# Performance work log

Hardware: AMD Instinct MI355X
Metric: run time of the kernel (lower is better)

Reference implementation:

```python
import jax, jax.numpy as jnp
import numpy as np

N = 50000
E = 400000
IN_DIM = 128
HID = 128
OUT = 128
HEADS = 8
NEG_SLOPE = 0.2  # PyG GATConv default
BN_EPS = 1e-5


def _gat_conv(x, W, a_src, a_dst, b, src, dst, concat):
    """PyG GATConv (eval): self-loops added by caller. x:[N,F], W:[F,H*C], a_*:[H,C]."""
    H, C = a_src.shape
    xW = (x @ W).reshape(N, H, C)                       # [N,H,C]
    es = jnp.sum(xW * a_src[None], axis=-1)             # [N,H]
    ed = jnp.sum(xW * a_dst[None], axis=-1)             # [N,H]
    e = jax.nn.leaky_relu(es[src] + ed[dst], NEG_SLOPE) # [E,H]
    m = jax.ops.segment_max(e, dst, num_segments=N)     # softmax over incoming edges per dst
    ex = jnp.exp(e - m[dst])
    denom = jax.ops.segment_sum(ex, dst, num_segments=N)
    alpha = ex / denom[dst]                             # [E,H]
    out = jax.ops.segment_sum(xW[src] * alpha[:, :, None], dst, num_segments=N)  # [N,H,C]
    out = out.reshape(N, H * C) if concat else out.mean(axis=1)
    return out + b


def _bn_eval(h, g, be, rm, rv):
    return (h - rm) * jax.lax.rsqrt(rv + BN_EPS) * g + be


def setup_inputs() -> dict:
    key = jax.random.key(0)
    ks = jax.random.split(key, 20)
    C1 = HID // HEADS
    f32 = jnp.float32
    inp = {
        "x": jax.random.normal(ks[0], (N, IN_DIM), dtype=f32),
        "edge_index": jax.random.randint(ks[1], (2, E), 0, N, dtype=jnp.int64),
        # GAT layer 1 (in->hid, 8 heads, concat)
        "W1": jax.random.normal(ks[2], (IN_DIM, HEADS * C1), dtype=f32) * 0.05,
        "a_src1": jax.random.normal(ks[3], (HEADS, C1), dtype=f32) * 0.05,
        "a_dst1": jax.random.normal(ks[4], (HEADS, C1), dtype=f32) * 0.05,
        "b1": jnp.zeros((HEADS * C1,), dtype=f32),
        # GAT layer 2 (hid->hid, 8 heads, concat)
        "W2": jax.random.normal(ks[5], (HID, HEADS * C1), dtype=f32) * 0.05,
        "a_src2": jax.random.normal(ks[6], (HEADS, C1), dtype=f32) * 0.05,
        "a_dst2": jax.random.normal(ks[7], (HEADS, C1), dtype=f32) * 0.05,
        "b2": jnp.zeros((HEADS * C1,), dtype=f32),
        # GAT layer 3 (hid->out, 1 head, no concat)
        "W3": jax.random.normal(ks[8], (HID, OUT), dtype=f32) * 0.05,
        "a_src3": jax.random.normal(ks[9], (1, OUT), dtype=f32) * 0.05,
        "a_dst3": jax.random.normal(ks[10], (1, OUT), dtype=f32) * 0.05,
        "b3": jnp.zeros((OUT,), dtype=f32),
        # residual linears
        "R1w": jax.random.normal(ks[11], (IN_DIM, HID), dtype=f32) * 0.05,
        "R1b": jnp.zeros((HID,), dtype=f32),
        "R2w": jax.random.normal(ks[12], (HID, HID), dtype=f32) * 0.05,
        "R2b": jnp.zeros((HID,), dtype=f32),
        "R3w": jax.random.normal(ks[13], (HID, OUT), dtype=f32) * 0.05,
        "R3b": jnp.zeros((OUT,), dtype=f32),
        # batch norms (eval mode: running stats)
        "g1": jnp.ones((HID,), dtype=f32), "be1": jnp.zeros((HID,), dtype=f32),
        "rm1": jnp.zeros((HID,), dtype=f32), "rv1": jnp.ones((HID,), dtype=f32),
        "g2": jnp.ones((HID,), dtype=f32), "be2": jnp.zeros((HID,), dtype=f32),
        "rm2": jnp.zeros((HID,), dtype=f32), "rv2": jnp.ones((HID,), dtype=f32),
    }
    return inp


def reference(x, edge_index, W1, a_src1, a_dst1, b1, W2, a_src2, a_dst2, b2,
              W3, a_src3, a_dst3, b3, R1w, R1b, R2w, R2b, R3w, R3b,
              g1, be1, rm1, rv1, g2, be2, rm2, rv2):
    # PyG GATConv adds self-loops by default
    loops = jnp.arange(N, dtype=edge_index.dtype)
    src = jnp.concatenate([edge_index[0], loops])
    dst = jnp.concatenate([edge_index[1], loops])

    h = _gat_conv(x, W1, a_src1, a_dst1, b1, src, dst, concat=True) + (x @ R1w + R1b)
    h1 = jax.nn.relu(_bn_eval(h, g1, be1, rm1, rv1))  # dropout identity in eval

    h = _gat_conv(h1, W2, a_src2, a_dst2, b2, src, dst, concat=True) + (h1 @ R2w + R2b)
    h2 = jax.nn.relu(_bn_eval(h, g2, be2, rm2, rv2))

    out = _gat_conv(h2, W3, a_src3, a_dst3, b3, src, dst, concat=False) + (h2 @ R3w + R3b)
    return out
```

## Files before the change

### kernel.cpp

```cpp
#include <hip/hip_runtime.h>
#include <hip/hip_bf16.h>
#include <type_traits>

typedef __hip_bfloat16 bf16;
typedef __hip_bfloat162 bf162;
typedef short v8s __attribute__((ext_vector_type(8)));
typedef short v4s __attribute__((ext_vector_type(4)));
typedef float v4f __attribute__((ext_vector_type(4)));

#define CAP 64

__device__ __forceinline__ float lrelu(float x) { return x > 0.f ? x : 0.2f * x; }
__device__ __forceinline__ float b2f(bf16 v) { return __bfloat162float(v); }

__global__ void k_preW(const float* __restrict__ s0, const float* __restrict__ s1,
                       const float* __restrict__ s2, const float* __restrict__ s3,
                       const float* __restrict__ s4, const float* __restrict__ s5,
                       const float* __restrict__ as1, const float* __restrict__ ad1,
                       const float* __restrict__ as2, const float* __restrict__ ad2,
                       const float* __restrict__ as3, const float* __restrict__ ad3,
                       const float* b1, const float* R1b, const float* g1, const float* be1,
                       const float* rm1, const float* rv1,
                       const float* b2, const float* R2b, const float* g2, const float* be2,
                       const float* rm2, const float* rv2,
                       const float* b3, const float* R3b,
                       bf16* __restrict__ wt, float* __restrict__ prm,
                       int* __restrict__ cnt, int N) {
    int b = blockIdx.x;
    int t = threadIdx.x;
    if (b >= 7) {
        int n4 = N * 4;
        int base = ((b - 7) * 256 + t) * 4;
        int4 z = {0, 0, 0, 0};
#pragma unroll
        for (int k = 0; k < 4; ++k)
            if (base + k < n4) ((int4*)cnt)[base + k] = z;
        return;
    }
    if (b == 6) {
        int c = t;
        if (c < 128) {
            float s1v = g1[c] * rsqrtf(rv1[c] + 1e-5f);
            prm[c]       = b1[c] + R1b[c];
            prm[128 + c] = s1v;
            prm[256 + c] = be1[c] - rm1[c] * s1v;
            float s2v = g2[c] * rsqrtf(rv2[c] + 1e-5f);
            prm[384 + c] = b2[c] + R2b[c];
            prm[512 + c] = s2v;
            prm[640 + c] = be2[c] - rm2[c] * s2v;
            prm[768 + c] = b3[c] + R3b[c];
        }
        return;
    }
    const float* src;
    switch (b) {
        case 0: src = s0; break; case 1: src = s1; break; case 2: src = s2; break;
        case 3: src = s3; break; case 4: src = s4; break; default: src = s5; break;
    }
    bf16* dst = wt + (size_t)b * 18432;
    for (int i = t; i < 16384; i += 256) {
        int k = i >> 7, n = i & 127;
        dst[n * 128 + k] = __float2bfloat16(src[i]);
    }
    if ((b & 1) == 0) {
        int layer = b >> 1;
        if (layer < 2) {
            const float* asr = (layer == 0) ? as1 : as2;
            const float* ads = (layer == 0) ? ad1 : ad2;
            for (int i = t; i < 2048; i += 256) {
                int row = i >> 7, k = i & 127, h = row & 7;
                const float* av = (row < 8) ? asr : ads;
                float s = 0.f;
#pragma unroll
                for (int c = 0; c < 16; ++c) s += src[k * 128 + h * 16 + c] * av[h * 16 + c];
                dst[(128 + row) * 128 + k] = __float2bfloat16(s);
            }
        } else {
            for (int i = t; i < 2048; i += 256) {
                int row = i >> 7, k = i & 127;
                float s = 0.f;
                if (row == 0 || row == 8) {
                    const float* av = (row == 0) ? as3 : ad3;
                    for (int c = 0; c < 128; ++c) s += src[k * 128 + c] * av[c];
                }
                dst[(128 + row) * 128 + k] = __float2bfloat16(s);
            }
        }
    } else {
        for (int i = t; i < 2048; i += 256)
            dst[16384 + i] = __float2bfloat16(0.f);
    }
}

template <typename T>
__device__ __forceinline__ void gemm_body(const T* __restrict__ A,
                                          const bf16* __restrict__ BT0, const bf16* __restrict__ BT1,
                                          bf16* __restrict__ O0, bf16* __restrict__ O1,
                                          float* __restrict__ esed, float* __restrict__ es,
                                          float* __restrict__ ed,
                                          int mode, int nrows, int job, int ntiles,
                                          bf16* Bsh) {
    const int y = (job >= ntiles) ? 1 : 0;
    const int tile = y ? job - ntiles : job;
    const bf16* BT = y ? BT1 : BT0;
    bf16* O = y ? O1 : O0;
    const int t = threadIdx.x;
    const int rowbase = tile * 128;
    const int wave = t >> 6, lane = t & 63, quad = lane >> 4, l16 = lane & 15;

    int gr[2], gc[2];
    gr[0] = rowbase + wave * 32 + l16; gc[0] = gr[0] < nrows ? gr[0] : nrows - 1;
    gr[1] = gr[0] + 16;                gc[1] = gr[1] < nrows ? gr[1] : nrows - 1;
    v8s afr[2][4];
    if constexpr (std::is_same<T, float>::value) {
#pragma unroll
        for (int rt = 0; rt < 2; ++rt) {
            const float* ar = A + (size_t)gc[rt] * 128 + quad * 8;
#pragma unroll
            for (int kit = 0; kit < 4; ++kit) {
                float4 u = *(const float4*)(ar + kit * 32);
                float4 w = *(const float4*)(ar + kit * 32 + 4);
                union { bf16 h[8]; v8s v; } tmp;
                tmp.h[0] = __float2bfloat16(u.x); tmp.h[1] = __float2bfloat16(u.y);
                tmp.h[2] = __float2bfloat16(u.z); tmp.h[3] = __float2bfloat16(u.w);
                tmp.h[4] = __float2bfloat16(w.x); tmp.h[5] = __float2bfloat16(w.y);
                tmp.h[6] = __float2bfloat16(w.z); tmp.h[7] = __float2bfloat16(w.w);
                afr[rt][kit] = tmp.v;
            }
        }
    } else {
#pragma unroll
        for (int rt = 0; rt < 2; ++rt) {
            const bf16* ar = A + (size_t)gc[rt] * 128 + quad * 8;
#pragma unroll
            for (int kit = 0; kit < 4; ++kit)
                afr[rt][kit] = *(const v8s*)(ar + kit * 32);
        }
    }

    for (int s = t; s < 288; s += 256) {
        int r = s >> 1, hf = s & 1;
        const float4* bsrc = (const float4*)(BT + r * 128 + hf * 64);
#pragma unroll
        for (int j = 0; j < 8; ++j) {
            int c = hf * 8 + j, cp = c ^ (r & 7);
            *(float4*)(&Bsh[r * 128 + cp * 8]) = bsrc[j];
        }
    }
    __syncthreads();

    v4f acc[2][9];
#pragma unroll
    for (int i = 0; i < 2; ++i)
#pragma unroll
        for (int j = 0; j < 9; ++j) acc[i][j] = (v4f){0.f, 0.f, 0.f, 0.f};
#pragma unroll
    for (int kit = 0; kit < 4; ++kit) {
        v8s bfr[9];
#pragma unroll
        for (int ct = 0; ct < 9; ++ct) {
            int nn = ct * 16 + l16;
            int cp = (kit * 4 + quad) ^ (nn & 7);
            bfr[ct] = *(const v8s*)(&Bsh[nn * 128 + cp * 8]);
        }
#pragma unroll
        for (int rt = 0; rt < 2; ++rt)
#pragma unroll
            for (int ct = 0; ct < 9; ++ct)
                acc[rt][ct] = __builtin_amdgcn_mfma_f32_16x16x32_bf16(bfr[ct], afr[rt][kit], acc[rt][ct], 0, 0, 0);
    }

#pragma unroll
    for (int rt = 0; rt < 2; ++rt) {
        if (gr[rt] < nrows) {
            bf16* orow = O + (size_t)gr[rt] * 128 + quad * 4;
#pragma unroll
            for (int ct = 0; ct < 8; ++ct) {
                union { bf16 h[4]; v4s v; } pk;
#pragma unroll
                for (int r = 0; r < 4; ++r) pk.h[r] = __float2bfloat16(acc[rt][ct][r]);
                *(v4s*)(orow + ct * 16) = pk.v;
            }
            if (mode == 1 && y == 0) {
                *(v4f*)(esed + (size_t)gr[rt] * 16 + quad * 4) = acc[rt][8];
            } else if (mode == 2 && y == 0) {
                if (quad == 0) es[gr[rt]] = acc[rt][8][0];
                else if (quad == 2) ed[gr[rt]] = acc[rt][8][0];
            }
        }
    }
}

__global__ void k_fillgemm(const float* __restrict__ A,
                           const bf16* __restrict__ BT0, const bf16* __restrict__ BT1,
                           bf16* __restrict__ O0, bf16* __restrict__ O1,
                           float* __restrict__ esed, float* __restrict__ es, float* __restrict__ ed,
                           int nrows, int ntiles, int fb,
                           const int* __restrict__ ei, int* __restrict__ cnt,
                           int* __restrict__ csr, int E) {
    __shared__ bf16 Bsh[144 * 128];
    const int nb = 2 * ntiles + fb;
    const int b = blockIdx.x;
    const int f0 = (int)(((long)b * fb) / nb);
    const int f1 = (int)(((long)(b + 1) * fb) / nb);
    if (f1 > f0) {
        int base = f0 * 1024 + threadIdx.x * 4;
        if (base >= E) return;
        if (((E & 3) == 0) && base + 3 < E) {
            int4 s4 = *(const int4*)(ei + base);
            int4 d4 = *(const int4*)(ei + E + base);
            int p0 = atomicAdd(&cnt[(size_t)d4.x * 16], 1);
            int p1 = atomicAdd(&cnt[(size_t)d4.y * 16], 1);
            int p2 = atomicAdd(&cnt[(size_t)d4.z * 16], 1);
            int p3 = atomicAdd(&cnt[(size_t)d4.w * 16], 1);
            if (p0 < CAP) csr[d4.x * CAP + p0] = s4.x;
            if (p1 < CAP) csr[d4.y * CAP + p1] = s4.y;
            if (p2 < CAP) csr[d4.z * CAP + p2] = s4.z;
            if (p3 < CAP) csr[d4.w * CAP + p3] = s4.w;
        } else {
            for (int i = base; i < E && i < base + 4; ++i) {
                int d = ei[E + i];
                int pos = atomicAdd(&cnt[(size_t)d * 16], 1);
                if (pos < CAP) csr[d * CAP + pos] = ei[i];
            }
        }
        return;
    }
    gemm_body<float>(A, BT0, BT1, O0, O1, esed, es, ed, 1, nrows, b - f0, ntiles, Bsh);
}

__global__ void k_gemm(const bf16* __restrict__ A,
                       const bf16* __restrict__ BT0, const bf16* __restrict__ BT1,
                       bf16* __restrict__ O0, bf16* __restrict__ O1,
                       float* __restrict__ esed, float* __restrict__ es, float* __restrict__ ed,
                       int mode, int nrows, int ntiles) {
    __shared__ bf16 Bsh[144 * 128];
    gemm_body<bf16>(A, BT0, BT1, O0, O1, esed, es, ed, mode, nrows, blockIdx.x, ntiles, Bsh);
}

__global__ void k_agg8(const bf16* __restrict__ xW, const float* __restrict__ esed,
                       const int* __restrict__ cnt, const int* __restrict__ csr,
                       const bf16* __restrict__ rres, const float* __restrict__ prm,
                       bf16* __restrict__ hout, int n) {
    int wave = threadIdx.x >> 6, lane = threadIdx.x & 63;
    int node = blockIdx.x * 4 + wave;
    if (node >= n) return;
    const int g = lane >> 4, l16 = lane & 15;
    const int c0 = l16 * 8;
    const int hc = l16 >> 1;
    const int he = lane & 7;
    float edw = esed[(size_t)node * 16 + 8 + he];
    float wselfh = __expf(lrelu(esed[(size_t)node * 16 + he] + edw));
    float acc[8]; float den = 0.f;
    v8s rv;
#pragma unroll
    for (int i = 0; i < 8; ++i) acc[i] = 0.f;
    {
        float ws = __shfl(wselfh, hc);
        if (g == 0) {
            rv = *(const v8s*)(rres + (size_t)node * 128 + c0);
            v8s xv = *(const v8s*)(xW + (size_t)node * 128 + c0);
            const bf16* xb = (const bf16*)&xv;
            den = ws;
#pragma unroll
            for (int i = 0; i < 8; ++i) acc[i] = ws * b2f(xb[i]);
        }
    }
    int deg = cnt[(size_t)node * 16]; if (deg > CAP) deg = CAP;
    const int* bucket = csr + (size_t)node * CAP;
    int idx = (lane < deg) ? bucket[lane] : node;
    for (int sub = 0; sub * 8 < deg; ++sub) {
        int j0 = sub * 8 + g, j1 = sub * 8 + 4 + g;
        int sv0 = __shfl(idx, j0);
        int sv1 = __shfl(idx, j1);
        v8s xv0 = *(const v8s*)(xW + (size_t)sv0 * 128 + c0);
        v8s xv1 = *(const v8s*)(xW + (size_t)sv1 * 128 + c0);
        int e = sub * 8 + (lane >> 3);
        int sidx = __shfl(idx, e);
        float esv = esed[(size_t)sidx * 16 + he];
        float w = (e < deg) ? __expf(lrelu(esv + edw)) : 0.f;
        float w0 = __shfl(w, g * 8 + hc);
        float w1 = __shfl(w, (4 + g) * 8 + hc);
        const bf16* xb0 = (const bf16*)&xv0;
        const bf16* xb1 = (const bf16*)&xv1;
        den += w0 + w1;
#pragma unroll
        for (int i = 0; i < 8; ++i) acc[i] += w0 * b2f(xb0[i]) + w1 * b2f(xb1[i]);
    }
    den += __shfl_xor(den, 16); den += __shfl_xor(den, 32);
#pragma unroll
    for (int i = 0; i < 8; ++i) {
        acc[i] += __shfl_xor(acc[i], 16);
        acc[i] += __shfl_xor(acc[i], 32);
    }
    if (g == 0) {
        float inv = 1.f / den;
        const bf16* rb = (const bf16*)&rv;
        bf16 outv[8];
#pragma unroll
        for (int i = 0; i < 8; ++i) {
            int c = c0 + i;
            float v = acc[i] * inv + prm[c] + b2f(rb[i]);
            v = fmaxf(v * prm[128 + c] + prm[256 + c], 0.f);
            outv[i] = __float2bfloat16(v);
        }
        *(v8s*)(hout + (size_t)node * 128 + c0) = *(v8s*)outv;
    }
}

__global__ void k_agg1(const bf16* __restrict__ xW, const float* __restrict__ es,
                       const float* __restrict__ ed,
                       const int* __restrict__ cnt, const int* __restrict__ csr,
                       const bf16* __restrict__ rres, const float* __restrict__ bias,
                       float* __restrict__ out, int n) {
    int wave = threadIdx.x >> 6, lane = threadIdx.x & 63;
    int node = blockIdx.x * 4 + wave;
    if (node >= n) return;
    const int g = lane >> 4, l16 = lane & 15;
    const int c0 = l16 * 8;
    float edv = ed[node];
    float wself = __expf(lrelu(es[node] + edv));
    float acc[8]; float den = 0.f;
    v8s rv;
#pragma unroll
    for (int i = 0; i < 8; ++i) acc[i] = 0.f;
    if (g == 0) {
        rv = *(const v8s*)(rres + (size_t)node * 128 + c0);
        v8s xv = *(const v8s*)(xW + (size_t)node * 128 + c0);
        const bf16* xb = (const bf16*)&xv;
        den = wself;
#pragma unroll
        for (int i = 0; i < 8; ++i) acc[i] = wself * b2f(xb[i]);
    }
    int deg = cnt[(size_t)node * 16]; if (deg > CAP) deg = CAP;
    const int* bucket = csr + (size_t)node * CAP;
    int idx = (lane < deg) ? bucket[lane] : node;
    float w = (lane < deg) ? __expf(lrelu(es[idx] + edv)) : 0.f;
    for (int j = 0; j < deg; j += 4) {
        int jl = j + g;
        int sv = __shfl(idx, jl);
        float wj = __shfl(w, jl);
        if (jl >= deg) wj = 0.f;
        v8s xv = *(const v8s*)(xW + (size_t)sv * 128 + c0);
        const bf16* xb = (const bf16*)&xv;
        den += wj;
#pragma unroll
        for (int i = 0; i < 8; ++i) acc[i] += wj * b2f(xb[i]);
    }
    den += __shfl_xor(den, 16); den += __shfl_xor(den, 32);
#pragma unroll
    for (int i = 0; i < 8; ++i) {
        acc[i] += __shfl_xor(acc[i], 16);
        acc[i] += __shfl_xor(acc[i], 32);
    }
    if (g == 0) {
        float inv = 1.f / den;
        const bf16* rb = (const bf16*)&rv;
        float ov[8];
#pragma unroll
        for (int i = 0; i < 8; ++i)
            ov[i] = acc[i] * inv + bias[c0 + i] + b2f(rb[i]);
        float4 o0, o1;
        o0.x = ov[0]; o0.y = ov[1]; o0.z = ov[2]; o0.w = ov[3];
        o1.x = ov[4]; o1.y = ov[5]; o1.z = ov[6]; o1.w = ov[7];
        *(float4*)(out + (size_t)node * 128 + c0) = o0;
        *(float4*)(out + (size_t)node * 128 + c0 + 4) = o1;
    }
}

extern "C" void kernel_launch(void* const* d_in, const int* in_sizes, int n_in,
                              void* d_out, int out_size, void* d_ws, size_t ws_size,
                              hipStream_t stream) {
    const float* x   = (const float*)d_in[0];
    const int*   ei  = (const int*)d_in[1];
    const float* W1  = (const float*)d_in[2];
    const float* as1 = (const float*)d_in[3];
    const float* ad1 = (const float*)d_in[4];
    const float* b1  = (const float*)d_in[5];
    const float* W2  = (const float*)d_in[6];
    const float* as2 = (const float*)d_in[7];
    const float* ad2 = (const float*)d_in[8];
    const float* b2  = (const float*)d_in[9];
    const float* W3  = (const float*)d_in[10];
    const float* as3 = (const float*)d_in[11];
    const float* ad3 = (const float*)d_in[12];
    const float* b3  = (const float*)d_in[13];
    const float* R1w = (const float*)d_in[14];
    const float* R1b = (const float*)d_in[15];
    const float* R2w = (const float*)d_in[16];
    const float* R2b = (const float*)d_in[17];
    const float* R3w = (const float*)d_in[18];
    const float* R3b = (const float*)d_in[19];
    const float* g1  = (const float*)d_in[20];
    const float* be1 = (const float*)d_in[21];
    const float* rm1 = (const float*)d_in[22];
    const float* rv1 = (const float*)d_in[23];
    const float* g2  = (const float*)d_in[24];
    const float* be2 = (const float*)d_in[25];
    const float* rm2 = (const float*)d_in[26];
    const float* rv2 = (const float*)d_in[27];

    const int N = in_sizes[0] / 128;
    const int E = in_sizes[1] / 2;

    char* p = (char*)d_ws;
    size_t off = 0;
    auto alloc = [&](size_t b) { void* r = p + off; off = (off + b + 255) & ~(size_t)255; return r; };
    int*   cnt  = (int*)alloc((size_t)N * 16 * 4);
    int*   csr  = (int*)alloc((size_t)N * CAP * 4);
    bf16*  WT   = (bf16*)alloc((size_t)6 * 18432 * 2);
    float* prm  = (float*)alloc(896 * 4);
    float* esed = (float*)alloc((size_t)N * 16 * 4);
    float* es   = (float*)alloc((size_t)N * 4);
    float* ed   = (float*)alloc((size_t)N * 4);
    bf16*  xW   = (bf16*)alloc((size_t)N * 128 * 2);
    bf16*  rres = (bf16*)alloc((size_t)N * 128 * 2);
    bf16*  hA   = (bf16*)alloc((size_t)N * 128 * 2);
    bf16*  hB   = (bf16*)alloc((size_t)N * 128 * 2);
    (void)ws_size; (void)n_in; (void)out_size;

    const int gx = (N + 127) / 128;
    const int nw = (N + 3) / 4;
    const int fb = (E + 1023) / 1024;
    const int zb = (N * 4 + 1023) / 1024;

    k_preW<<<7 + zb, 256, 0, stream>>>(W1, R1w, W2, R2w, W3, R3w,
                                       as1, ad1, as2, ad2, as3, ad3,
                                       b1, R1b, g1, be1, rm1, rv1,
                                       b2, R2b, g2, be2, rm2, rv2, b3, R3b,
                                       WT, prm, cnt, N);
    k_fillgemm<<<2 * gx + fb, 256, 0, stream>>>(x, WT, WT + 18432, xW, rres, esed, es, ed,
                                                N, gx, fb, ei, cnt, csr, E);
    k_agg8<<<nw, 256, 0, stream>>>(xW, esed, cnt, csr, rres, prm, hA, N);
    k_gemm<<<2 * gx, 256, 0, stream>>>(hA, WT + 2 * 18432, WT + 3 * 18432, xW, rres, esed, es, ed, 1, N, gx);
    k_agg8<<<nw, 256, 0, stream>>>(xW, esed, cnt, csr, rres, prm + 384, hB, N);
    k_gemm<<<2 * gx, 256, 0, stream>>>(hB, WT + 4 * 18432, WT + 5 * 18432, xW, rres, esed, es, ed, 2, N, gx);
    k_agg1<<<nw, 256, 0, stream>>>(xW, es, ed, cnt, csr, rres, prm + 768, (float*)d_out, N);
}
```

Baseline: 335.0 us.

## Stage GEMM output through LDS for coalesced row stores; reorder fill/gemm blocks

```diff
diff --git a/kernel.cpp b/kernel.cpp
--- a/kernel.cpp
+++ b/kernel.cpp
@@ -170,17 +170,41 @@
                 acc[rt][ct] = __builtin_amdgcn_mfma_f32_16x16x32_bf16(bfr[ct], afr[rt][kit], acc[rt][ct], 0, 0, 0);
     }
 
+    __syncthreads();
+
+    bf16* Tw = Bsh + wave * 4096;
+#pragma unroll
+    for (int rt = 0; rt < 2; ++rt) {
+        bf16* trow = Tw + (rt * 16 + l16) * 128;
+#pragma unroll
+        for (int ct = 0; ct < 8; ++ct) {
+            union { bf16 h[4]; v4s v; } pk;
+#pragma unroll
+            for (int r = 0; r < 4; ++r) pk.h[r] = __float2bfloat16(acc[rt][ct][r]);
+            int e = (ct * 16 + quad * 4 + l16 * 8) & 127;
+            *(v4s*)(trow + e) = pk.v;
+        }
+    }
+#pragma unroll
+    for (int o = 0; o < 2; ++o) {
+        int r32 = o * 16 + (lane >> 2);
+        int q4 = lane & 3;
+        int grow = rowbase + wave * 32 + r32;
+        const bf16* trow = Tw + r32 * 128;
+        int rot = (r32 & 15) * 8;
+        if (grow < nrows) {
+            bf16* orow = O + (size_t)grow * 128;
+#pragma unroll
+            for (int j = 0; j < 4; ++j) {
+                int c = q4 * 8 + j * 32;
+                int pc = (c + rot) & 127;
+                *(float4*)(orow + c) = *(const float4*)(trow + pc);
+            }
+        }
+    }
 #pragma unroll
     for (int rt = 0; rt < 2; ++rt) {
         if (gr[rt] < nrows) {
-            bf16* orow = O + (size_t)gr[rt] * 128 + quad * 4;
-#pragma unroll
-            for (int ct = 0; ct < 8; ++ct) {
-                union { bf16 h[4]; v4s v; } pk;
-#pragma unroll
-                for (int r = 0; r < 4; ++r) pk.h[r] = __float2bfloat16(acc[rt][ct][r]);
-                *(v4s*)(orow + ct * 16) = pk.v;
-            }
             if (mode == 1 && y == 0) {
                 *(v4f*)(esed + (size_t)gr[rt] * 16 + quad * 4) = acc[rt][8];
             } else if (mode == 2 && y == 0) {
@@ -195,38 +219,35 @@
                            const bf16* __restrict__ BT0, const bf16* __restrict__ BT1,
                            bf16* __restrict__ O0, bf16* __restrict__ O1,
                            float* __restrict__ esed, float* __restrict__ es, float* __restrict__ ed,
-                           int nrows, int ntiles, int fb,
+                           int nrows, int ntiles,
                            const int* __restrict__ ei, int* __restrict__ cnt,
                            int* __restrict__ csr, int E) {
-    __shared__ bf16 Bsh[144 * 128];
-    const int nb = 2 * ntiles + fb;
-    const int b = blockIdx.x;
-    const int f0 = (int)(((long)b * fb) / nb);
-    const int f1 = (int)(((long)(b + 1) * fb) / nb);
-    if (f1 > f0) {
-        int base = f0 * 1024 + threadIdx.x * 4;
-        if (base >= E) return;
-        if (((E & 3) == 0) && base + 3 < E) {
-            int4 s4 = *(const int4*)(ei + base);
-            int4 d4 = *(const int4*)(ei + E + base);
-            int p0 = atomicAdd(&cnt[(size_t)d4.x * 16], 1);
-            int p1 = atomicAdd(&cnt[(size_t)d4.y * 16], 1);
-            int p2 = atomicAdd(&cnt[(size_t)d4.z * 16], 1);
-            int p3 = atomicAdd(&cnt[(size_t)d4.w * 16], 1);
-            if (p0 < CAP) csr[d4.x * CAP + p0] = s4.x;
-            if (p1 < CAP) csr[d4.y * CAP + p1] = s4.y;
-            if (p2 < CAP) csr[d4.z * CAP + p2] = s4.z;
-            if (p3 < CAP) csr[d4.w * CAP + p3] = s4.w;
-        } else {
-            for (int i = base; i < E && i < base + 4; ++i) {
-                int d = ei[E + i];
-                int pos = atomicAdd(&cnt[(size_t)d * 16], 1);
-                if (pos < CAP) csr[d * CAP + pos] = ei[i];
-            }
-        }
+    __shared__ __align__(16) bf16 Bsh[144 * 128];
+    const int njobs = 2 * ntiles;
+    if (blockIdx.x < njobs) {
+        gemm_body<float>(A, BT0, BT1, O0, O1, esed, es, ed, 1, nrows, blockIdx.x, ntiles, Bsh);
         return;
     }
-    gemm_body<float>(A, BT0, BT1, O0, O1, esed, es, ed, 1, nrows, b - f0, ntiles, Bsh);
+    int base = (blockIdx.x - njobs) * 1024 + threadIdx.x * 4;
+    if (base >= E) return;
+    if (((E & 3) == 0) && base + 3 < E) {
+        int4 s4 = *(const int4*)(ei + base);
+        int4 d4 = *(const int4*)(ei + E + base);
+        int p0 = atomicAdd(&cnt[(size_t)d4.x * 16], 1);
+        int p1 = atomicAdd(&cnt[(size_t)d4.y * 16], 1);
+        int p2 = atomicAdd(&cnt[(size_t)d4.z * 16], 1);
+        int p3 = atomicAdd(&cnt[(size_t)d4.w * 16], 1);
+        if (p0 < CAP) csr[d4.x * CAP + p0] = s4.x;
+        if (p1 < CAP) csr[d4.y * CAP + p1] = s4.y;
+        if (p2 < CAP) csr[d4.z * CAP + p2] = s4.z;
+        if (p3 < CAP) csr[d4.w * CAP + p3] = s4.w;
+    } else {
+        for (int i = base; i < E && i < base + 4; ++i) {
+            int d = ei[E + i];
+            int pos = atomicAdd(&cnt[(size_t)d * 16], 1);
+            if (pos < CAP) csr[d * CAP + pos] = ei[i];
+        }
+    }
 }
 
 __global__ void k_gemm(const bf16* __restrict__ A,
@@ -234,7 +255,7 @@
                        bf16* __restrict__ O0, bf16* __restrict__ O1,
                        float* __restrict__ esed, float* __restrict__ es, float* __restrict__ ed,
                        int mode, int nrows, int ntiles) {
-    __shared__ bf16 Bsh[144 * 128];
+    __shared__ __align__(16) bf16 Bsh[144 * 128];
     gemm_body<bf16>(A, BT0, BT1, O0, O1, esed, es, ed, mode, nrows, blockIdx.x, ntiles, Bsh);
 }
 
@@ -430,7 +451,7 @@
                                        b2, R2b, g2, be2, rm2, rv2, b3, R3b,
                                        WT, prm, cnt, N);
     k_fillgemm<<<2 * gx + fb, 256, 0, stream>>>(x, WT, WT + 18432, xW, rres, esed, es, ed,
-                                                N, gx, fb, ei, cnt, csr, E);
+                                                N, gx, ei, cnt, csr, E);
     k_agg8<<<nw, 256, 0, stream>>>(xW, esed, cnt, csr, rres, prm, hA, N);
     k_gemm<<<2 * gx, 256, 0, stream>>>(hA, WT + 2 * 18432, WT + 3 * 18432, xW, rres, esed, es, ed, 1, N, gx);
     k_agg8<<<nw, 256, 0, stream>>>(xW, esed, cnt, csr, rres, prm + 384, hB, N);
```

After: 314.8 us. 6.0% less time.
